# Optimization experiments

Measured on AMD Instinct MI355X. Metric: run time of the kernel, lower is better.

The kernel has to match this reference:

```python
import jax, jax.numpy as jnp
import numpy as np

D = 8        # shared feature dim (sIN=sOUT=yDIM=sPROJ)
H = 64       # MLP hidden
EPS = 1e-5


def setup_inputs() -> dict:
    key = jax.random.key(0)
    ks = jax.random.split(key, 12)
    s = lambda fan_in: 1.0 / np.sqrt(fan_in)
    inp = {
        "x": jax.random.normal(ks[0], (16384, D), jnp.float32),
        "y": jax.random.normal(ks[1], (4096, D), jnp.float32),
        # attention projections (torch Linear weight: [out, in], no bias)
        "Wq": jax.random.uniform(ks[2], (D, D), jnp.float32, -s(D), s(D)),
        "Wk": jax.random.uniform(ks[3], (D, D), jnp.float32, -s(D), s(D)),
        "Wv": jax.random.uniform(ks[4], (D, D), jnp.float32, -s(D), s(D)),
        # MLP [8, 64, 64, 8]: Linear-ReLU-Linear-ReLU-Linear
        "W1": jax.random.uniform(ks[5], (H, D), jnp.float32, -s(D), s(D)),
        "b1": jax.random.uniform(ks[6], (H,), jnp.float32, -s(D), s(D)),
        "W2": jax.random.uniform(ks[7], (H, H), jnp.float32, -s(H), s(H)),
        "b2": jax.random.uniform(ks[8], (H,), jnp.float32, -s(H), s(H)),
        "W3": jax.random.uniform(ks[9], (D, H), jnp.float32, -s(H), s(H)),
        "b3": jax.random.uniform(ks[10], (D,), jnp.float32, -s(H), s(H)),
        # shared LayerNorm(sOUT) params
        "ln_w": jnp.ones((D,), jnp.float32),
        "ln_b": jnp.zeros((D,), jnp.float32),
    }
    return inp


def _layer_norm(t, w, b):
    mu = jnp.mean(t, axis=-1, keepdims=True)
    var = jnp.var(t, axis=-1, keepdims=True)
    return (t - mu) * jax.lax.rsqrt(var + EPS) * w + b


def _smooth_softmax(m):
    # softmax over keys (dim 1) blended with 0.1*relu, renormalized
    s = jax.nn.softmax(m, axis=1)
    num = jax.nn.relu(m) * 0.1 + s
    return num / jnp.sum(num, axis=1, keepdims=True)


def reference(x, y, Wq, Wk, Wv, W1, b1, W2, b2, W3, b3, ln_w, ln_b):
    z1 = _layer_norm(x, ln_w, ln_b)          # [N, D]
    w = _layer_norm(y, ln_w, ln_b)           # [M, D]
    XQ = z1 @ Wq.T                           # [N, D]
    YK = w @ Wk.T                            # [M, D]
    YV = w @ Wv.T                            # [M, D]
    M = (XQ @ YK.T) / np.sqrt(YK.shape[1]).astype(np.float32)  # [N, M]
    M = _smooth_softmax(M)
    z1 = M @ YV + x                          # residual 1
    z2 = _layer_norm(z1, ln_w, ln_b)
    z2 = jax.nn.relu(z2 @ W1.T + b1)
    z2 = jax.nn.relu(z2 @ W2.T + b2)
    z2 = z2 @ W3.T + b3
    return z2 + z1                           # residual 2
```

## Files before the change

### kernel.cpp

```cpp
#include <hip/hip_runtime.h>
#include <hip/hip_bf16.h>

#define NQ 16384
#define NKV 4096
#define EPSF 1e-5f
#define SCALE2 0.5100604576761344f
#define C1 0.06931471805599453f

typedef float f32x4 __attribute__((ext_vector_type(4)));
typedef short s16x4 __attribute__((ext_vector_type(4)));

union U2S4 { uint2 u; s16x4 s; };

#if __has_builtin(__builtin_amdgcn_mfma_f32_16x16x16bf16_1k)
#define MFMA16(a, b, c) __builtin_amdgcn_mfma_f32_16x16x16bf16_1k((a), (b), (c), 0, 0, 0)
#else
static __device__ __forceinline__ f32x4 mfma16_asm(s16x4 a, s16x4 b, f32x4 c) {
    asm volatile("v_mfma_f32_16x16x16_bf16 %0, %1, %2, %0" : "+v"(c) : "v"(a), "v"(b));
    return c;
}
#define MFMA16(a, b, c) mfma16_asm((a), (b), (c))
#endif

#if __has_builtin(__builtin_amdgcn_exp2f)
#define EXP2F(x) __builtin_amdgcn_exp2f(x)
#else
#define EXP2F(x) exp2f(x)
#endif

__device__ __forceinline__ unsigned int pk_bf16(float a, float b) {
    unsigned int r;
    asm("v_cvt_pk_bf16_f32 %0, %1, %2" : "=v"(r) : "v"(a), "v"(b));
    return r;
}

__global__ void preproc_kernel(const float* __restrict__ x, const float* __restrict__ y,
                               const float* __restrict__ Wq, const float* __restrict__ Wk,
                               const float* __restrict__ Wv, const float* __restrict__ ln_w,
                               const float* __restrict__ ln_b,
                               ushort* __restrict__ QH, ushort* __restrict__ KH,
                               ushort* __restrict__ VTT) {
    int row = blockIdx.x * blockDim.x + threadIdx.x;
    if (row >= NQ + NKV) return;
    bool is_x = row < NQ;
    const float* src = is_x ? (x + (size_t)row * 8) : (y + (size_t)(row - NQ) * 8);
    float4 a = ((const float4*)src)[0];
    float4 b = ((const float4*)src)[1];
    float t[8] = {a.x,a.y,a.z,a.w,b.x,b.y,b.z,b.w};
    float mu = 0.f;
    #pragma unroll
    for (int i = 0; i < 8; i++) mu += t[i];
    mu *= 0.125f;
    float var = 0.f;
    #pragma unroll
    for (int i = 0; i < 8; i++) { float d = t[i] - mu; var += d * d; }
    var *= 0.125f;
    float rs = rsqrtf(var + EPSF);
    float z[8];
    #pragma unroll
    for (int i = 0; i < 8; i++) z[i] = (t[i] - mu) * rs * ln_w[i] + ln_b[i];

    if (is_x) {
        float o[8];
        #pragma unroll
        for (int oo = 0; oo < 8; oo++) {
            float acc = 0.f;
            #pragma unroll
            for (int i = 0; i < 8; i++) acc += Wq[oo*8+i] * z[i];
            o[oo] = acc;
        }
        uint4 lo, hi;
        lo.x = pk_bf16(o[0],o[1]); lo.y = pk_bf16(o[2],o[3]);
        lo.z = pk_bf16(o[4],o[5]); lo.w = pk_bf16(o[6],o[7]);
        hi.x = hi.y = hi.z = hi.w = 0u;
        uint4* dst = (uint4*)(QH + (size_t)row * 16);
        dst[0] = lo; dst[1] = hi;
    } else {
        int r = row - NQ;
        float ok[8], ov[8];
        #pragma unroll
        for (int oo = 0; oo < 8; oo++) {
            float ak = 0.f, av = 0.f;
            #pragma unroll
            for (int i = 0; i < 8; i++) { ak += Wk[oo*8+i]*z[i]; av += Wv[oo*8+i]*z[i]; }
            ok[oo] = ak * SCALE2; ov[oo] = av;
        }
        uint4 lo, hi;
        lo.x = pk_bf16(ok[0],ok[1]); lo.y = pk_bf16(ok[2],ok[3]);
        lo.z = pk_bf16(ok[4],ok[5]); lo.w = pk_bf16(ok[6],ok[7]);
        hi.x = hi.y = hi.z = hi.w = 0u;
        uint4* dst = (uint4*)(KH + (size_t)r * 16);
        dst[0] = lo; dst[1] = hi;

        ushort* vt = VTT + (size_t)(r >> 4) * 256 + (r & 15);
        #pragma unroll
        for (int d = 0; d < 8; d++) {
            unsigned int p = pk_bf16(ov[d], 0.f);
            vt[d * 16] = (ushort)(p & 0xFFFF);
        }
        vt[8 * 16] = 0x3F80;
        #pragma unroll
        for (int d = 9; d < 16; d++) vt[d * 16] = 0;
    }
}

__global__ __launch_bounds__(1024) void attn_kernel(
        const ushort* __restrict__ QH, const ushort* __restrict__ KH,
        const ushort* __restrict__ VTT, const float* __restrict__ x,
        float* __restrict__ Z1) {
    __shared__ f32x4 Le[16][2][48];
    __shared__ f32x4 Lr[16][2][48];

    const int tid  = threadIdx.x;
    const int w    = tid >> 6;
    const int lane = tid & 63;
    const int grp  = lane >> 4;
    const int qi   = lane & 15;
    const int q0   = blockIdx.x * 32;

    U2S4 qf0, qf1;
    qf0.u = *(const uint2*)(QH + (size_t)(q0 + qi) * 16 + 4 * grp);
    qf1.u = *(const uint2*)(QH + (size_t)(q0 + 16 + qi) * 16 + 4 * grp);

    const ushort* kp = KH  + (size_t)(w * 16) * 256 + qi * 16 + 4 * grp;
    const ushort* vp = VTT + (size_t)(w * 16) * 256 + qi * 16 + 4 * grp;

    f32x4 ae0 = {0.f,0.f,0.f,0.f}, ar0 = {0.f,0.f,0.f,0.f};
    f32x4 ae1 = {0.f,0.f,0.f,0.f}, ar1 = {0.f,0.f,0.f,0.f};

    U2S4 k0, v0, k1, v1, k2, v2;
    k0.u = *(const uint2*)kp;        v0.u = *(const uint2*)vp;
    k1.u = *(const uint2*)(kp+256);  v1.u = *(const uint2*)(vp+256);
    kp += 512; vp += 512;

    #pragma unroll 8
    for (int t = 0; t < 16; t++) {
        k2.u = *(const uint2*)kp;  v2.u = *(const uint2*)vp;
        kp += 256; vp += 256;

        f32x4 s0 = MFMA16(k0.s, qf0.s, ((f32x4){0.f,0.f,0.f,0.f}));
        f32x4 s1 = MFMA16(k0.s, qf1.s, ((f32x4){0.f,0.f,0.f,0.f}));

        float e00 = EXP2F(s0[0]), e01 = EXP2F(s0[1]), e02 = EXP2F(s0[2]), e03 = EXP2F(s0[3]);
        float e10 = EXP2F(s1[0]), e11 = EXP2F(s1[1]), e12 = EXP2F(s1[2]), e13 = EXP2F(s1[3]);
        float r00 = fmaxf(s0[0],0.f), r01 = fmaxf(s0[1],0.f), r02 = fmaxf(s0[2],0.f), r03 = fmaxf(s0[3],0.f);
        float r10 = fmaxf(s1[0],0.f), r11 = fmaxf(s1[1],0.f), r12 = fmaxf(s1[2],0.f), r13 = fmaxf(s1[3],0.f);

        U2S4 pe0, pr0, pe1, pr1;
        pe0.u.x = pk_bf16(e00,e01); pe0.u.y = pk_bf16(e02,e03);
        pe1.u.x = pk_bf16(e10,e11); pe1.u.y = pk_bf16(e12,e13);
        pr0.u.x = pk_bf16(r00,r01); pr0.u.y = pk_bf16(r02,r03);
        pr1.u.x = pk_bf16(r10,r11); pr1.u.y = pk_bf16(r12,r13);

        ae0 = MFMA16(v0.s, pe0.s, ae0);
        ar0 = MFMA16(v0.s, pr0.s, ar0);
        ae1 = MFMA16(v0.s, pe1.s, ae1);
        ar1 = MFMA16(v0.s, pr1.s, ar1);

        k0 = k1; v0 = v1;
        k1 = k2; v1 = v2;
    }

    if (grp < 3) {
        Le[w][0][lane] = ae0; Le[w][1][lane] = ae1;
        Lr[w][0][lane] = ar0; Lr[w][1][lane] = ar1;
    }
    __syncthreads();

    if (tid < 64) {
        const int qloc = tid & 31, g = tid >> 5;
        const int j = qloc >> 4, q = qloc & 15;
        f32x4 Ae = {0.f,0.f,0.f,0.f}, Ar = {0.f,0.f,0.f,0.f};
        float Z = 0.f, R = 0.f;
        #pragma unroll
        for (int w2 = 0; w2 < 16; w2++) {
            Ae += Le[w2][j][g*16+q];
            Ar += Lr[w2][j][g*16+q];
            Z  += Le[w2][j][32+q][0];
            R  += Lr[w2][j][32+q][0];
        }
        float iz  = 1.0f / Z;
        float den = 1.0f / (C1 * R + 1.0f);
        float4 xr = *(const float4*)(x + (size_t)(q0 + qloc) * 8 + 4 * g);
        float4 o;
        o.x = (C1 * Ar[0] + Ae[0] * iz) * den + xr.x;
        o.y = (C1 * Ar[1] + Ae[1] * iz) * den + xr.y;
        o.z = (C1 * Ar[2] + Ae[2] * iz) * den + xr.z;
        o.w = (C1 * Ar[3] + Ae[3] * iz) * den + xr.w;
        *(float4*)(Z1 + (size_t)(q0 + qloc) * 8 + 4 * g) = o;
    }
}

__global__ __launch_bounds__(256) void mlp_kernel(
        const float* __restrict__ Z1,
        const float* __restrict__ W1, const float* __restrict__ b1,
        const float* __restrict__ W2, const float* __restrict__ b2,
        const float* __restrict__ W3, const float* __restrict__ b3,
        const float* __restrict__ ln_w, const float* __restrict__ ln_b,
        float* __restrict__ out) {
    __shared__ float W1s[512], W2s[64*68], W3s[512], b1s[64], b2s[64], b3s[8], lw[8], lb[8];
    for (int i = threadIdx.x; i < 512; i += 256) { W1s[i] = W1[i]; W3s[i] = W3[i]; }
    for (int i = threadIdx.x; i < 4096; i += 256) W2s[(i >> 6) * 68 + (i & 63)] = W2[i];
    if (threadIdx.x < 64) { b1s[threadIdx.x] = b1[threadIdx.x]; b2s[threadIdx.x] = b2[threadIdx.x]; }
    if (threadIdx.x < 8) { b3s[threadIdx.x] = b3[threadIdx.x]; lw[threadIdx.x] = ln_w[threadIdx.x]; lb[threadIdx.x] = ln_b[threadIdx.x]; }
    __syncthreads();

    int gid = blockIdx.x * 256 + threadIdx.x;
    int row = gid >> 3;
    int og  = threadIdx.x & 7;

    const float4* zp = (const float4*)(Z1 + (size_t)row * 8);
    float4 a = zp[0], b = zp[1];
    float z1r[8] = {a.x,a.y,a.z,a.w,b.x,b.y,b.z,b.w};
    float mu = 0.f;
    #pragma unroll
    for (int i = 0; i < 8; i++) mu += z1r[i];
    mu *= 0.125f;
    float var = 0.f;
    #pragma unroll
    for (int i = 0; i < 8; i++) { float d = z1r[i] - mu; var += d * d; }
    var *= 0.125f;
    float rs = rsqrtf(var + EPSF);
    float z2[8];
    #pragma unroll
    for (int i = 0; i < 8; i++) z2[i] = (z1r[i] - mu) * rs * lw[i] + lb[i];

    float h[64];
    #pragma unroll
    for (int o = 0; o < 64; o++) {
        float acc = b1s[o];
        #pragma unroll
        for (int i = 0; i < 8; i++) acc += W1s[o*8+i] * z2[i];
        h[o] = fmaxf(acc, 0.f);
    }

    float oacc[8];
    #pragma unroll
    for (int d = 0; d < 8; d++) oacc[d] = 0.f;
    #pragma unroll
    for (int oo = 0; oo < 8; oo++) {
        int o = og + 8 * oo;
        float a0 = 0.f, a1 = 0.f, a2 = 0.f, a3 = 0.f;
        const float4* w2r = (const float4*)(W2s + o * 68);
        #pragma unroll
        for (int i4 = 0; i4 < 16; i4++) {
            float4 wv = w2r[i4];
            a0 += wv.x * h[4*i4];   a1 += wv.y * h[4*i4+1];
            a2 += wv.z * h[4*i4+2]; a3 += wv.w * h[4*i4+3];
        }
        float act = fmaxf(b2s[o] + ((a0 + a1) + (a2 + a3)), 0.f);
        #pragma unroll
        for (int d = 0; d < 8; d++) oacc[d] += W3s[d*64+o] * act;
    }

    #pragma unroll
    for (int m = 1; m <= 4; m <<= 1) {
        #pragma unroll
        for (int d = 0; d < 8; d++) oacc[d] += __shfl_xor(oacc[d], m);
    }
    if (og == 0) {
        float4* op = (float4*)(out + (size_t)row * 8);
        op[0] = make_float4(oacc[0]+b3s[0]+z1r[0], oacc[1]+b3s[1]+z1r[1],
                            oacc[2]+b3s[2]+z1r[2], oacc[3]+b3s[3]+z1r[3]);
        op[1] = make_float4(oacc[4]+b3s[4]+z1r[4], oacc[5]+b3s[5]+z1r[5],
                            oacc[6]+b3s[6]+z1r[6], oacc[7]+b3s[7]+z1r[7]);
    }
}

extern "C" void kernel_launch(void* const* d_in, const int* in_sizes, int n_in,
                              void* d_out, int out_size, void* d_ws, size_t ws_size,
                              hipStream_t stream) {
    const float* x   = (const float*)d_in[0];
    const float* y   = (const float*)d_in[1];
    const float* Wq  = (const float*)d_in[2];
    const float* Wk  = (const float*)d_in[3];
    const float* Wv  = (const float*)d_in[4];
    const float* W1  = (const float*)d_in[5];
    const float* b1  = (const float*)d_in[6];
    const float* W2  = (const float*)d_in[7];
    const float* b2  = (const float*)d_in[8];
    const float* W3  = (const float*)d_in[9];
    const float* b3  = (const float*)d_in[10];
    const float* lnw = (const float*)d_in[11];
    const float* lnb = (const float*)d_in[12];

    char* ws = (char*)d_ws;
    ushort* QH  = (ushort*)ws;
    ushort* KH  = (ushort*)(ws + 524288);
    ushort* VTT = (ushort*)(ws + 655360);
    float*  Z1  = (float*)(ws + 786432);
    float* out = (float*)d_out;

    preproc_kernel<<<(NQ + NKV + 255) / 256, 256, 0, stream>>>(x, y, Wq, Wk, Wv, lnw, lnb, QH, KH, VTT);
    attn_kernel<<<NQ / 32, 1024, 0, stream>>>(QH, KH, VTT, x, Z1);
    mlp_kernel<<<(NQ * 8) / 256, 256, 0, stream>>>(Z1, W1, b1, W2, b2, W3, b3, lnw, lnb, out);
}
```

Baseline: 35.98 us.

## Fuse Q projection, attention and MLP into one kernel per 64-query tile

Result: slower. 57.45 us (+59.7%).

```diff
diff --git a/kernel.cpp b/kernel.cpp
--- a/kernel.cpp
+++ b/kernel.cpp
@@ -34,16 +34,14 @@
     return r;
 }
 
-__global__ void preproc_kernel(const float* __restrict__ x, const float* __restrict__ y,
-                               const float* __restrict__ Wq, const float* __restrict__ Wk,
-                               const float* __restrict__ Wv, const float* __restrict__ ln_w,
-                               const float* __restrict__ ln_b,
-                               ushort* __restrict__ QH, ushort* __restrict__ KH,
-                               ushort* __restrict__ VTT) {
-    int row = blockIdx.x * blockDim.x + threadIdx.x;
-    if (row >= NQ + NKV) return;
-    bool is_x = row < NQ;
-    const float* src = is_x ? (x + (size_t)row * 8) : (y + (size_t)(row - NQ) * 8);
+__global__ __launch_bounds__(64) void kv_kernel(
+        const float* __restrict__ y, const float* __restrict__ Wk,
+        const float* __restrict__ Wv, const float* __restrict__ ln_w,
+        const float* __restrict__ ln_b,
+        ushort* __restrict__ KH, ushort* __restrict__ VTT) {
+    int r = blockIdx.x * 64 + threadIdx.x;
+    if (r >= NKV) return;
+    const float* src = y + (size_t)r * 8;
     float4 a = ((const float4*)src)[0];
     float4 b = ((const float4*)src)[1];
     float t[8] = {a.x,a.y,a.z,a.w,b.x,b.y,b.z,b.w};
@@ -60,7 +58,70 @@
     #pragma unroll
     for (int i = 0; i < 8; i++) z[i] = (t[i] - mu) * rs * ln_w[i] + ln_b[i];
 
-    if (is_x) {
+    float ok[8], ov[8];
+    #pragma unroll
+    for (int oo = 0; oo < 8; oo++) {
+        float ak = 0.f, av = 0.f;
+        #pragma unroll
+        for (int i = 0; i < 8; i++) { ak += Wk[oo*8+i]*z[i]; av += Wv[oo*8+i]*z[i]; }
+        ok[oo] = ak * SCALE2; ov[oo] = av;
+    }
+    uint4 lo, hi;
+    lo.x = pk_bf16(ok[0],ok[1]); lo.y = pk_bf16(ok[2],ok[3]);
+    lo.z = pk_bf16(ok[4],ok[5]); lo.w = pk_bf16(ok[6],ok[7]);
+    hi.x = hi.y = hi.z = hi.w = 0u;
+    uint4* dst = (uint4*)(KH + (size_t)r * 16);
+    dst[0] = lo; dst[1] = hi;
+
+    ushort* vt = VTT + (size_t)(r >> 4) * 256 + (r & 15);
+    #pragma unroll
+    for (int d = 0; d < 8; d++) {
+        unsigned int p = pk_bf16(ov[d], 0.f);
+        vt[d * 16] = (ushort)(p & 0xFFFF);
+    }
+    vt[8 * 16] = 0x3F80;
+    #pragma unroll
+    for (int d = 9; d < 16; d++) vt[d * 16] = 0;
+}
+
+__global__ __launch_bounds__(512) void fused_kernel(
+        const float* __restrict__ x,  const float* __restrict__ Wq,
+        const float* __restrict__ ln_w, const float* __restrict__ ln_b,
+        const ushort* __restrict__ KH, const ushort* __restrict__ VTT,
+        const float* __restrict__ W1, const float* __restrict__ b1,
+        const float* __restrict__ W2, const float* __restrict__ b2,
+        const float* __restrict__ W3, const float* __restrict__ b3,
+        float* __restrict__ out) {
+    __shared__ ushort Qlds[64][16];
+    __shared__ f32x4 Le[8][4][48];
+    __shared__ f32x4 Lr[8][4][48];
+    __shared__ float Z1lds[64][8];
+    __shared__ float W3s[512];
+
+    const int tid  = threadIdx.x;
+    const int w    = tid >> 6;
+    const int lane = tid & 63;
+    const int grp  = lane >> 4;
+    const int qi   = lane & 15;
+    const int q0   = blockIdx.x * 64;
+
+    if (tid < 64) {
+        const float* src = x + (size_t)(q0 + tid) * 8;
+        float4 a = ((const float4*)src)[0];
+        float4 b = ((const float4*)src)[1];
+        float t[8] = {a.x,a.y,a.z,a.w,b.x,b.y,b.z,b.w};
+        float mu = 0.f;
+        #pragma unroll
+        for (int i = 0; i < 8; i++) mu += t[i];
+        mu *= 0.125f;
+        float var = 0.f;
+        #pragma unroll
+        for (int i = 0; i < 8; i++) { float d = t[i] - mu; var += d * d; }
+        var *= 0.125f;
+        float rs = rsqrtf(var + EPSF);
+        float z[8];
+        #pragma unroll
+        for (int i = 0; i < 8; i++) z[i] = (t[i] - mu) * rs * ln_w[i] + ln_b[i];
         float o[8];
         #pragma unroll
         for (int oo = 0; oo < 8; oo++) {
@@ -73,107 +134,71 @@
         lo.x = pk_bf16(o[0],o[1]); lo.y = pk_bf16(o[2],o[3]);
         lo.z = pk_bf16(o[4],o[5]); lo.w = pk_bf16(o[6],o[7]);
         hi.x = hi.y = hi.z = hi.w = 0u;
-        uint4* dst = (uint4*)(QH + (size_t)row * 16);
-        dst[0] = lo; dst[1] = hi;
-    } else {
-        int r = row - NQ;
-        float ok[8], ov[8];
-        #pragma unroll
-        for (int oo = 0; oo < 8; oo++) {
-            float ak = 0.f, av = 0.f;
-            #pragma unroll
-            for (int i = 0; i < 8; i++) { ak += Wk[oo*8+i]*z[i]; av += Wv[oo*8+i]*z[i]; }
-            ok[oo] = ak * SCALE2; ov[oo] = av;
-        }
-        uint4 lo, hi;
-        lo.x = pk_bf16(ok[0],ok[1]); lo.y = pk_bf16(ok[2],ok[3]);
-        lo.z = pk_bf16(ok[4],ok[5]); lo.w = pk_bf16(ok[6],ok[7]);
-        hi.x = hi.y = hi.z = hi.w = 0u;
-        uint4* dst = (uint4*)(KH + (size_t)r * 16);
-        dst[0] = lo; dst[1] = hi;
-
-        ushort* vt = VTT + (size_t)(r >> 4) * 256 + (r & 15);
-        #pragma unroll
-        for (int d = 0; d < 8; d++) {
-            unsigned int p = pk_bf16(ov[d], 0.f);
-            vt[d * 16] = (ushort)(p & 0xFFFF);
-        }
-        vt[8 * 16] = 0x3F80;
-        #pragma unroll
-        for (int d = 9; d < 16; d++) vt[d * 16] = 0;
-    }
-}
-
-__global__ __launch_bounds__(1024) void attn_kernel(
-        const ushort* __restrict__ QH, const ushort* __restrict__ KH,
-        const ushort* __restrict__ VTT, const float* __restrict__ x,
-        float* __restrict__ Z1) {
-    __shared__ f32x4 Le[16][2][48];
-    __shared__ f32x4 Lr[16][2][48];
-
-    const int tid  = threadIdx.x;
-    const int w    = tid >> 6;
-    const int lane = tid & 63;
-    const int grp  = lane >> 4;
-    const int qi   = lane & 15;
-    const int q0   = blockIdx.x * 32;
-
-    U2S4 qf0, qf1;
-    qf0.u = *(const uint2*)(QH + (size_t)(q0 + qi) * 16 + 4 * grp);
-    qf1.u = *(const uint2*)(QH + (size_t)(q0 + 16 + qi) * 16 + 4 * grp);
-
-    const ushort* kp = KH  + (size_t)(w * 16) * 256 + qi * 16 + 4 * grp;
-    const ushort* vp = VTT + (size_t)(w * 16) * 256 + qi * 16 + 4 * grp;
-
-    f32x4 ae0 = {0.f,0.f,0.f,0.f}, ar0 = {0.f,0.f,0.f,0.f};
-    f32x4 ae1 = {0.f,0.f,0.f,0.f}, ar1 = {0.f,0.f,0.f,0.f};
+        uint4* qdst = (uint4*)&Qlds[tid][0];
+        qdst[0] = lo; qdst[1] = hi;
+    } else if (tid < 192) {
+        int i = (tid - 64) * 4;
+        *(float4*)&W3s[i] = *(const float4*)&W3[i];
+    }
+    __syncthreads();
+
+    U2S4 qf[4];
+    #pragma unroll
+    for (int f = 0; f < 4; f++)
+        qf[f].u = *(const uint2*)&Qlds[16*f + qi][4*grp];
+
+    const ushort* kp = KH  + (size_t)(w * 32) * 256 + qi * 16 + 4 * grp;
+    const ushort* vp = VTT + (size_t)(w * 32) * 256 + qi * 16 + 4 * grp;
+
+    f32x4 ae[4], ar[4];
+    #pragma unroll
+    for (int f = 0; f < 4; f++) { ae[f] = (f32x4){0,0,0,0}; ar[f] = (f32x4){0,0,0,0}; }
 
     U2S4 k0, v0, k1, v1, k2, v2;
     k0.u = *(const uint2*)kp;        v0.u = *(const uint2*)vp;
     k1.u = *(const uint2*)(kp+256);  v1.u = *(const uint2*)(vp+256);
     kp += 512; vp += 512;
 
-    #pragma unroll 8
-    for (int t = 0; t < 16; t++) {
+    #pragma unroll 2
+    for (int t = 0; t < 32; t++) {
         k2.u = *(const uint2*)kp;  v2.u = *(const uint2*)vp;
         kp += 256; vp += 256;
 
-        f32x4 s0 = MFMA16(k0.s, qf0.s, ((f32x4){0.f,0.f,0.f,0.f}));
-        f32x4 s1 = MFMA16(k0.s, qf1.s, ((f32x4){0.f,0.f,0.f,0.f}));
-
-        float e00 = EXP2F(s0[0]), e01 = EXP2F(s0[1]), e02 = EXP2F(s0[2]), e03 = EXP2F(s0[3]);
-        float e10 = EXP2F(s1[0]), e11 = EXP2F(s1[1]), e12 = EXP2F(s1[2]), e13 = EXP2F(s1[3]);
-        float r00 = fmaxf(s0[0],0.f), r01 = fmaxf(s0[1],0.f), r02 = fmaxf(s0[2],0.f), r03 = fmaxf(s0[3],0.f);
-        float r10 = fmaxf(s1[0],0.f), r11 = fmaxf(s1[1],0.f), r12 = fmaxf(s1[2],0.f), r13 = fmaxf(s1[3],0.f);
-
-        U2S4 pe0, pr0, pe1, pr1;
-        pe0.u.x = pk_bf16(e00,e01); pe0.u.y = pk_bf16(e02,e03);
-        pe1.u.x = pk_bf16(e10,e11); pe1.u.y = pk_bf16(e12,e13);
-        pr0.u.x = pk_bf16(r00,r01); pr0.u.y = pk_bf16(r02,r03);
-        pr1.u.x = pk_bf16(r10,r11); pr1.u.y = pk_bf16(r12,r13);
-
-        ae0 = MFMA16(v0.s, pe0.s, ae0);
-        ar0 = MFMA16(v0.s, pr0.s, ar0);
-        ae1 = MFMA16(v0.s, pe1.s, ae1);
-        ar1 = MFMA16(v0.s, pr1.s, ar1);
+        f32x4 s[4];
+        #pragma unroll
+        for (int f = 0; f < 4; f++)
+            s[f] = MFMA16(k0.s, qf[f].s, ((f32x4){0.f,0.f,0.f,0.f}));
+
+        #pragma unroll
+        for (int f = 0; f < 4; f++) {
+            float e0 = EXP2F(s[f][0]), e1 = EXP2F(s[f][1]);
+            float e2 = EXP2F(s[f][2]), e3 = EXP2F(s[f][3]);
+            float r0 = fmaxf(s[f][0],0.f), r1 = fmaxf(s[f][1],0.f);
+            float r2 = fmaxf(s[f][2],0.f), r3 = fmaxf(s[f][3],0.f);
+            U2S4 pe, pr;
+            pe.u.x = pk_bf16(e0,e1); pe.u.y = pk_bf16(e2,e3);
+            pr.u.x = pk_bf16(r0,r1); pr.u.y = pk_bf16(r2,r3);
+            ae[f] = MFMA16(v0.s, pe.s, ae[f]);
+            ar[f] = MFMA16(v0.s, pr.s, ar[f]);
+        }
 
         k0 = k1; v0 = v1;
         k1 = k2; v1 = v2;
     }
 
     if (grp < 3) {
-        Le[w][0][lane] = ae0; Le[w][1][lane] = ae1;
-        Lr[w][0][lane] = ar0; Lr[w][1][lane] = ar1;
+        #pragma unroll
+        for (int f = 0; f < 4; f++) { Le[w][f][lane] = ae[f]; Lr[w][f][lane] = ar[f]; }
     }
     __syncthreads();
 
-    if (tid < 64) {
-        const int qloc = tid & 31, g = tid >> 5;
+    if (tid < 128) {
+        const int g = tid >> 6, qloc = tid & 63;
         const int j = qloc >> 4, q = qloc & 15;
-        f32x4 Ae = {0.f,0.f,0.f,0.f}, Ar = {0.f,0.f,0.f,0.f};
+        f32x4 Ae = {0,0,0,0}, Ar = {0,0,0,0};
         float Z = 0.f, R = 0.f;
         #pragma unroll
-        for (int w2 = 0; w2 < 16; w2++) {
+        for (int w2 = 0; w2 < 8; w2++) {
             Ae += Le[w2][j][g*16+q];
             Ar += Lr[w2][j][g*16+q];
             Z  += Le[w2][j][32+q][0];
@@ -182,36 +207,19 @@
         float iz  = 1.0f / Z;
         float den = 1.0f / (C1 * R + 1.0f);
         float4 xr = *(const float4*)(x + (size_t)(q0 + qloc) * 8 + 4 * g);
-        float4 o;
-        o.x = (C1 * Ar[0] + Ae[0] * iz) * den + xr.x;
-        o.y = (C1 * Ar[1] + Ae[1] * iz) * den + xr.y;
-        o.z = (C1 * Ar[2] + Ae[2] * iz) * den + xr.z;
-        o.w = (C1 * Ar[3] + Ae[3] * iz) * den + xr.w;
-        *(float4*)(Z1 + (size_t)(q0 + qloc) * 8 + 4 * g) = o;
-    }
-}
-
-__global__ __launch_bounds__(256) void mlp_kernel(
-        const float* __restrict__ Z1,
-        const float* __restrict__ W1, const float* __restrict__ b1,
-        const float* __restrict__ W2, const float* __restrict__ b2,
-        const float* __restrict__ W3, const float* __restrict__ b3,
-        const float* __restrict__ ln_w, const float* __restrict__ ln_b,
-        float* __restrict__ out) {
-    __shared__ float W1s[512], W2s[64*68], W3s[512], b1s[64], b2s[64], b3s[8], lw[8], lb[8];
-    for (int i = threadIdx.x; i < 512; i += 256) { W1s[i] = W1[i]; W3s[i] = W3[i]; }
-    for (int i = threadIdx.x; i < 4096; i += 256) W2s[(i >> 6) * 68 + (i & 63)] = W2[i];
-    if (threadIdx.x < 64) { b1s[threadIdx.x] = b1[threadIdx.x]; b2s[threadIdx.x] = b2[threadIdx.x]; }
-    if (threadIdx.x < 8) { b3s[threadIdx.x] = b3[threadIdx.x]; lw[threadIdx.x] = ln_w[threadIdx.x]; lb[threadIdx.x] = ln_b[threadIdx.x]; }
+        Z1lds[qloc][4*g+0] = (C1 * Ar[0] + Ae[0] * iz) * den + xr.x;
+        Z1lds[qloc][4*g+1] = (C1 * Ar[1] + Ae[1] * iz) * den + xr.y;
+        Z1lds[qloc][4*g+2] = (C1 * Ar[2] + Ae[2] * iz) * den + xr.z;
+        Z1lds[qloc][4*g+3] = (C1 * Ar[3] + Ae[3] * iz) * den + xr.w;
+    }
     __syncthreads();
 
-    int gid = blockIdx.x * 256 + threadIdx.x;
-    int row = gid >> 3;
-    int og  = threadIdx.x & 7;
-
-    const float4* zp = (const float4*)(Z1 + (size_t)row * 8);
-    float4 a = zp[0], b = zp[1];
-    float z1r[8] = {a.x,a.y,a.z,a.w,b.x,b.y,b.z,b.w};
+    const int row = tid >> 3;
+    const int og  = tid & 7;
+
+    float z1r[8];
+    #pragma unroll
+    for (int i = 0; i < 8; i++) z1r[i] = Z1lds[row][i];
     float mu = 0.f;
     #pragma unroll
     for (int i = 0; i < 8; i++) mu += z1r[i];
@@ -220,17 +228,17 @@
     #pragma unroll
     for (int i = 0; i < 8; i++) { float d = z1r[i] - mu; var += d * d; }
     var *= 0.125f;
-    float rs = rsqrtf(var + EPSF);
+    float rs2 = rsqrtf(var + EPSF);
     float z2[8];
     #pragma unroll
-    for (int i = 0; i < 8; i++) z2[i] = (z1r[i] - mu) * rs * lw[i] + lb[i];
+    for (int i = 0; i < 8; i++) z2[i] = (z1r[i] - mu) * rs2 * ln_w[i] + ln_b[i];
 
     float h[64];
     #pragma unroll
     for (int o = 0; o < 64; o++) {
-        float acc = b1s[o];
-        #pragma unroll
-        for (int i = 0; i < 8; i++) acc += W1s[o*8+i] * z2[i];
+        float acc = b1[o];
+        #pragma unroll
+        for (int i = 0; i < 8; i++) acc += W1[o*8+i] * z2[i];
         h[o] = fmaxf(acc, 0.f);
     }
 
@@ -241,14 +249,14 @@
     for (int oo = 0; oo < 8; oo++) {
         int o = og + 8 * oo;
         float a0 = 0.f, a1 = 0.f, a2 = 0.f, a3 = 0.f;
-        const float4* w2r = (const float4*)(W2s + o * 68);
+        const float4* w2r = (const float4*)(W2 + o * 64);
         #pragma unroll
         for (int i4 = 0; i4 < 16; i4++) {
             float4 wv = w2r[i4];
             a0 += wv.x * h[4*i4];   a1 += wv.y * h[4*i4+1];
             a2 += wv.z * h[4*i4+2]; a3 += wv.w * h[4*i4+3];
         }
-        float act = fmaxf(b2s[o] + ((a0 + a1) + (a2 + a3)), 0.f);
+        float act = fmaxf(b2[o] + ((a0 + a1) + (a2 + a3)), 0.f);
         #pragma unroll
         for (int d = 0; d < 8; d++) oacc[d] += W3s[d*64+o] * act;
     }
@@ -259,11 +267,11 @@
         for (int d = 0; d < 8; d++) oacc[d] += __shfl_xor(oacc[d], m);
     }
     if (og == 0) {
-        float4* op = (float4*)(out + (size_t)row * 8);
-        op[0] = make_float4(oacc[0]+b3s[0]+z1r[0], oacc[1]+b3s[1]+z1r[1],
-                            oacc[2]+b3s[2]+z1r[2], oacc[3]+b3s[3]+z1r[3]);
-        op[1] = make_float4(oacc[4]+b3s[4]+z1r[4], oacc[5]+b3s[5]+z1r[5],
-                            oacc[6]+b3s[6]+z1r[6], oacc[7]+b3s[7]+z1r[7]);
+        float4* op = (float4*)(out + (size_t)(q0 + row) * 8);
+        op[0] = make_float4(oacc[0]+b3[0]+z1r[0], oacc[1]+b3[1]+z1r[1],
+                            oacc[2]+b3[2]+z1r[2], oacc[3]+b3[3]+z1r[3]);
+        op[1] = make_float4(oacc[4]+b3[4]+z1r[4], oacc[5]+b3[5]+z1r[5],
+                            oacc[6]+b3[6]+z1r[6], oacc[7]+b3[7]+z1r[7]);
     }
 }
 
@@ -285,13 +293,11 @@
     const float* lnb = (const float*)d_in[12];
 
     char* ws = (char*)d_ws;
-    ushort* QH  = (ushort*)ws;
-    ushort* KH  = (ushort*)(ws + 524288);
-    ushort* VTT = (ushort*)(ws + 655360);
-    float*  Z1  = (float*)(ws + 786432);
+    ushort* KH  = (ushort*)ws;
+    ushort* VTT = (ushort*)(ws + 131072);
     float* out = (float*)d_out;
 
-    preproc_kernel<<<(NQ + NKV + 255) / 256, 256, 0, stream>>>(x, y, Wq, Wk, Wv, lnw, lnb, QH, KH, VTT);
-    attn_kernel<<<NQ / 32, 1024, 0, stream>>>(QH, KH, VTT, x, Z1);
-    mlp_kernel<<<(NQ * 8) / 256, 256, 0, stream>>>(Z1, W1, b1, W2, b2, W3, b3, lnw, lnb, out);
-}
+    kv_kernel<<<NKV / 64, 64, 0, stream>>>(y, Wk, Wv, lnw, lnb, KH, VTT);
+    fused_kernel<<<NQ / 64, 512, 0, stream>>>(x, Wq, lnw, lnb, KH, VTT,
+                                              W1, b1, W2, b2, W3, b3, out);
+}
```
